# Optimization experiments

Hardware: AMD Instinct MI355X
Metric: run time of the kernel (lower is better)

The kernel has to match this reference:

```python
import jax, jax.numpy as jnp
import numpy as np

HEADS = 12
D_MODEL = 768
D_K = D_MODEL // HEADS


def setup_inputs() -> dict:
    key = jax.random.key(0)
    ks = jax.random.split(key, 5)
    B, S = 2, 2048
    scale = 1.0 / np.sqrt(D_MODEL)
    return {
        "q": jax.random.normal(ks[0], (B, S, D_MODEL), dtype=jnp.float32),
        "k": jax.random.normal(ks[1], (B, S, D_MODEL), dtype=jnp.float32),
        "v": jax.random.normal(ks[2], (B, S, D_MODEL), dtype=jnp.float32),
        "Wk": jax.random.normal(ks[3], (D_MODEL, D_MODEL), dtype=jnp.float32) * scale,
        "bk": jnp.zeros((D_MODEL,), dtype=jnp.float32),
        "Wo": jax.random.normal(ks[4], (D_MODEL, D_MODEL), dtype=jnp.float32) * scale,
        "bo": jnp.zeros((D_MODEL,), dtype=jnp.float32),
    }


def reference(q, k, v, Wk, bk, Wo, bo):
    B, S, _ = q.shape
    # NOTE: faithful to source bug: q, k, v ALL projected with k_linear.
    def proj(x):
        y = x @ Wk.T + bk                    # [B,S,D]
        return y.reshape(B, -1, HEADS, D_K).transpose(0, 2, 1, 3)  # [B,H,S,Dk]

    qh, kh, vh = proj(q), proj(k), proj(v)
    scores = jnp.einsum('bhsd,bhtd->bhst', qh, kh) / jnp.sqrt(jnp.float32(D_K))
    attn = jax.nn.softmax(scores, axis=-1)   # dropout is identity in eval
    out = jnp.einsum('bhst,bhtd->bhsd', attn, vh)
    concat = out.transpose(0, 2, 1, 3).reshape(B, -1, D_MODEL)
    return concat @ Wo.T + bo
```

## Files before the change

### kernel.cpp

```cpp
#include <hip/hip_runtime.h>
#include <hip/hip_bf16.h>
#include <stddef.h>

#define HEADS 12
#define DM 768
#define DK 64
#define SEQ 2048
#define NB 2
#define WSZ (DM * DM)
#define QSCALE 0.18033688011112043f

typedef __attribute__((ext_vector_type(8))) short short8;
typedef __attribute__((ext_vector_type(4))) float f32x4;
typedef __attribute__((ext_vector_type(16))) float f32x16;

#define MFMA16(A, B, C) __builtin_amdgcn_mfma_f32_16x16x32_bf16((A), (B), (C), 0, 0, 0)
#define MFMA32(A, B, C) __builtin_amdgcn_mfma_f32_32x32x16_bf16((A), (B), (C), 0, 0, 0)

__device__ __forceinline__ unsigned short f2bf(float x) {
  union { float f; unsigned u; } c;
  c.f = x;
  unsigned r = (c.u + 0x7FFFu + ((c.u >> 16) & 1u)) >> 16;
  return (unsigned short)r;
}
__device__ __forceinline__ float bf2f(unsigned short h) {
  union { float f; unsigned u; } c;
  c.u = ((unsigned)h) << 16;
  return c.f;
}

__device__ __forceinline__ void async16(const void* g, void* l) {
  __builtin_amdgcn_global_load_lds(
      (const __attribute__((address_space(1))) void*)g,
      (__attribute__((address_space(3))) void*)l, 16, 0, 0);
}

__device__ __forceinline__ void splitpk(float a, float b, unsigned& hu, unsigned& lu) {
  union { __hip_bfloat162 v; unsigned u; } c;
  c.v = __float22bfloat162_rn(make_float2(a, b));
  hu = c.u;
  const float ra = a - bf2f((unsigned short)(hu & 0xFFFFu));
  const float rb = b - bf2f((unsigned short)(hu >> 16));
  c.v = __float22bfloat162_rn(make_float2(ra, rb));
  lu = c.u;
}
__device__ __forceinline__ unsigned pk2bf(float a, float b) {
  union { __hip_bfloat162 v; unsigned u; } c;
  c.v = __float22bfloat162_rn(make_float2(a, b));
  return c.u;
}

__device__ __forceinline__ void pl32swap(unsigned& a, unsigned& b) {
  auto r = __builtin_amdgcn_permlane32_swap(a, b, false, false);
  a = r[0];
  b = r[1];
}


__global__ __launch_bounds__(256) void prep_split(
    const float* __restrict__ q, const float* __restrict__ k,
    const float* __restrict__ v, const float* __restrict__ Wk,
    const float* __restrict__ Wo, unsigned short* __restrict__ xq,
    unsigned short* __restrict__ xk, unsigned short* __restrict__ xv,
    unsigned short* __restrict__ wkh, unsigned short* __restrict__ wkl,
    unsigned short* __restrict__ woh, unsigned short* __restrict__ wol) {
  __shared__ __align__(16) unsigned short Lh[64 * 136];
  __shared__ __align__(16) unsigned short Ll[64 * 136];
  const int tid = threadIdx.x;
  int id = blockIdx.x;
  const float* S;
  unsigned short *H, *L = nullptr;
  int RT, RT16;
  if (id < 1152) {
    S = (id < 384) ? q : (id < 768) ? k : v;
    H = (id < 384) ? xq : (id < 768) ? xk : xv;
    id = id % 384; RT = 64; RT16 = 256;
  } else if (id < 1224) {
    S = Wk; H = wkh; L = wkl; id -= 1152; RT = 12; RT16 = 48;
  } else {
    S = Wo; H = woh; L = wol; id -= 1224; RT = 12; RT16 = 48;
  }
  const int rb = id % RT, kb = id / RT;
  const int mlane = tid >> 4;
  const int klane = (tid & 15) * 8;

#pragma unroll
  for (int rr = 0; rr < 4; ++rr) {
    const int m = rr * 16 + mlane;
    const float* src = &S[(size_t)(rb * 64 + m) * DM + kb * 128 + klane];
    float a[8];
    *(float4*)&a[0] = *(const float4*)&src[0];
    *(float4*)&a[4] = *(const float4*)&src[4];
    if (L) {
      unsigned hu[4], lu[4];
#pragma unroll
      for (int u = 0; u < 4; ++u) splitpk(a[2 * u], a[2 * u + 1], hu[u], lu[u]);
      *(uint4*)&Lh[m * 136 + klane] = *(uint4*)&hu[0];
      *(uint4*)&Ll[m * 136 + klane] = *(uint4*)&lu[0];
    } else {
      unsigned hu[4];
#pragma unroll
      for (int u = 0; u < 4; ++u) hu[u] = pk2bf(a[2 * u], a[2 * u + 1]);
      *(uint4*)&Lh[m * 136 + klane] = *(uint4*)&hu[0];
    }
  }
  __syncthreads();

  const int t = tid >> 4;
  const int ktp = t >> 2, mtp = t & 3;
  const size_t gt = ((size_t)(kb * 4 + ktp) * RT16 + (rb * 4 + mtp)) * 512;
#pragma unroll
  for (int i = 0; i < 4; ++i) {
    const int c = i * 16 + (tid & 15);
    const int lsrc = (mtp * 16 + (tid & 15)) * 136 + ktp * 32 + i * 8;
    *(uint4*)&H[gt + c * 8] = *(uint4*)&Lh[lsrc];
    if (L) *(uint4*)&L[gt + c * 8] = *(uint4*)&Ll[lsrc];
  }
}

__global__ __launch_bounds__(256, 3) void gemm_proj(
    const unsigned short* __restrict__ Xq, const unsigned short* __restrict__ Xk,
    const unsigned short* __restrict__ Xv, const unsigned short* __restrict__ Bh_,
    const unsigned short* __restrict__ Bl_, const float* __restrict__ bias,
    unsigned short* __restrict__ q_h, unsigned short* __restrict__ q_l,
    unsigned short* __restrict__ k_h, unsigned short* __restrict__ vt_h) {
  __shared__ __align__(16) unsigned short Ash[8 * 512];
  __shared__ __align__(16) unsigned short Bsh[6 * 512];
  __shared__ __align__(16) unsigned short Bsl[6 * 512];

  const int tid = threadIdx.x, z = blockIdx.z;
  const unsigned short* __restrict__ A = (z == 0) ? Xq : (z == 1) ? Xk : Xv;
  const int id = blockIdx.x;
  const int mt0 = (id & 31) * 8, nt0 = (id >> 5) * 6;
  const int lane = tid & 63, wv = tid >> 6;
  const int l15 = lane & 15, quad = lane >> 4;
  const int wm = (wv >> 1) * 4, wn = (wv & 1) * 3;
  const int lx = lane * 8;

  f32x4 acc[4][3];
#pragma unroll
  for (int i = 0; i < 4; ++i)
#pragma unroll
    for (int j = 0; j < 3; ++j) acc[i][j] = (f32x4){0.f, 0.f, 0.f, 0.f};

  for (int kt = 0; kt < 24; ++kt) {
    __syncthreads();
    async16(&A[((size_t)kt * 256 + mt0 + wv) * 512 + lx], &Ash[wv * 512]);
    async16(&A[((size_t)kt * 256 + mt0 + wv + 4) * 512 + lx], &Ash[(wv + 4) * 512]);
    async16(&Bh_[((size_t)kt * 48 + nt0 + wv) * 512 + lx], &Bsh[wv * 512]);
    async16(&Bl_[((size_t)kt * 48 + nt0 + wv) * 512 + lx], &Bsl[wv * 512]);
    if (wv < 2)
      async16(&Bh_[((size_t)kt * 48 + nt0 + 4 + wv) * 512 + lx], &Bsh[(4 + wv) * 512]);
    else
      async16(&Bl_[((size_t)kt * 48 + nt0 + 2 + wv) * 512 + lx], &Bsl[(2 + wv) * 512]);
    __syncthreads();

    short8 bh8[3], bl8[3];
#pragma unroll
    for (int nt = 0; nt < 3; ++nt) {
      bh8[nt] = *(const short8*)&Bsh[(wn + nt) * 512 + lx];
      bl8[nt] = *(const short8*)&Bsl[(wn + nt) * 512 + lx];
    }
#pragma unroll
    for (int mt = 0; mt < 4; ++mt) {
      const short8 ah8 = *(const short8*)&Ash[(wm + mt) * 512 + lx];
#pragma unroll
      for (int nt = 0; nt < 3; ++nt) {
        acc[mt][nt] = MFMA16(ah8, bh8[nt], acc[mt][nt]);
        acc[mt][nt] = MFMA16(ah8, bl8[nt], acc[mt][nt]);
      }
    }
  }

#pragma unroll
  for (int mt = 0; mt < 4; ++mt)
#pragma unroll
    for (int nt = 0; nt < 3; ++nt) {
      const int n = (nt0 + wn + nt) * 16 + l15;
      const float bv = bias[n];
      const int hh = n >> 6, dk = n & 63;
#pragma unroll
      for (int j = 0; j < 4; ++j) {
        const int m = (mt0 + wm + mt) * 16 + quad * 4 + j;
        const int b = m >> 11, t = m & 2047;
        const int bh = b * HEADS + hh;
        if (z == 0) {
          const float y = (acc[mt][nt][j] + bv) * QSCALE;
          const unsigned short yh = f2bf(y);
          const int a = (bh * SEQ + t) * DK + dk;
          q_h[a] = yh;
          q_l[a] = f2bf(y - bf2f(yh));
        } else if (z == 1) {
          const int a = bh * 131072 + (t >> 5) * 2048 + (dk >> 4) * 512 +
                        ((t & 31) + ((dk & 15) >> 3) * 32) * 8 + (dk & 7);
          k_h[a] = f2bf(acc[mt][nt][j] + bv);
        } else {
          const int a = bh * 131072 + (t >> 4) * 1024 + (dk >> 5) * 512 +
                        ((dk & 31) + ((t & 15) >> 3) * 32) * 8 + (t & 7);
          vt_h[a] = f2bf(acc[mt][nt][j] + bv);
        }
      }
    }
}

__global__ __launch_bounds__(256, 2) void gemm_out(
    const unsigned short* __restrict__ Ah_, const unsigned short* __restrict__ Al_,
    const unsigned short* __restrict__ Bh_, const unsigned short* __restrict__ Bl_,
    const float* __restrict__ bias, float* __restrict__ outF) {
  __shared__ __align__(16) unsigned short Ash[4 * 512];
  __shared__ __align__(16) unsigned short Asl[4 * 512];
  __shared__ __align__(16) unsigned short Bsh[6 * 512];
  __shared__ __align__(16) unsigned short Bsl[6 * 512];

  const int tid = threadIdx.x, id = blockIdx.x;
  const int mt0 = (id & 63) * 4, nt0 = (id >> 6) * 6;
  const int lane = tid & 63, wv = tid >> 6;
  const int l15 = lane & 15, quad = lane >> 4;
  const int wm = (wv >> 1) * 2, wn = (wv & 1) * 3;
  const int lx = lane * 8;

  f32x4 acc[2][3];
#pragma unroll
  for (int i = 0; i < 2; ++i)
#pragma unroll
    for (int j = 0; j < 3; ++j) acc[i][j] = (f32x4){0.f, 0.f, 0.f, 0.f};

  for (int kt = 0; kt < 24; ++kt) {
    __syncthreads();
    async16(&Ah_[((size_t)kt * 256 + mt0 + wv) * 512 + lx], &Ash[wv * 512]);
    async16(&Al_[((size_t)kt * 256 + mt0 + wv) * 512 + lx], &Asl[wv * 512]);
    async16(&Bh_[((size_t)kt * 48 + nt0 + wv) * 512 + lx], &Bsh[wv * 512]);
    async16(&Bl_[((size_t)kt * 48 + nt0 + wv) * 512 + lx], &Bsl[wv * 512]);
    if (wv < 2)
      async16(&Bh_[((size_t)kt * 48 + nt0 + 4 + wv) * 512 + lx], &Bsh[(4 + wv) * 512]);
    else
      async16(&Bl_[((size_t)kt * 48 + nt0 + 2 + wv) * 512 + lx], &Bsl[(2 + wv) * 512]);
    __syncthreads();

    short8 bh8[3], bl8[3];
#pragma unroll
    for (int nt = 0; nt < 3; ++nt) {
      bh8[nt] = *(const short8*)&Bsh[(wn + nt) * 512 + lx];
      bl8[nt] = *(const short8*)&Bsl[(wn + nt) * 512 + lx];
    }
#pragma unroll
    for (int mt = 0; mt < 2; ++mt) {
      const short8 ah8 = *(const short8*)&Ash[(wm + mt) * 512 + lx];
      const short8 al8 = *(const short8*)&Asl[(wm + mt) * 512 + lx];
#pragma unroll
      for (int nt = 0; nt < 3; ++nt) {
        acc[mt][nt] = MFMA16(ah8, bh8[nt], acc[mt][nt]);
        acc[mt][nt] = MFMA16(al8, bh8[nt], acc[mt][nt]);
        acc[mt][nt] = MFMA16(ah8, bl8[nt], acc[mt][nt]);
      }
    }
  }

#pragma unroll
  for (int mt = 0; mt < 2; ++mt)
#pragma unroll
    for (int nt = 0; nt < 3; ++nt) {
      const int n = (nt0 + wn + nt) * 16 + l15;
      const float bv = bias[n];
#pragma unroll
      for (int j = 0; j < 4; ++j) {
        const int m = (mt0 + wm + mt) * 16 + quad * 4 + j;
        outF[(size_t)m * DM + n] = acc[mt][nt][j] + bv;
      }
    }
}

__global__ __launch_bounds__(256, 3) void attn_mfma(
    const unsigned short* __restrict__ q_h, const unsigned short* __restrict__ q_l,
    const unsigned short* __restrict__ k_h, const unsigned short* __restrict__ vt_h,
    unsigned short* __restrict__ cch, unsigned short* __restrict__ ccl) {
  __shared__ __align__(16) union {
    unsigned short stage[32 * 512];
    float osh[64 * 64];
  } sm;
  __shared__ float Lred[4][32];

  const int tid = threadIdx.x, lane = tid & 63, wv = tid >> 6;
  const int l31 = lane & 31, hi = lane >> 5;
  const int qh = wv & 1, th = wv >> 1;
  const int id = blockIdx.x;
  const int bh = id % 24, q0 = (id / 24) << 6;
  const int lx = lane * 8;

  short8 Qf[4][2];
#pragma unroll
  for (int ks = 0; ks < 4; ++ks) {
    const int off = (bh * SEQ + q0 + qh * 32 + l31) * DK + ks * 16 + hi * 8;
    Qf[ks][0] = *(const short8*)&q_h[off];
    Qf[ks][1] = *(const short8*)&q_l[off];
  }

  f32x16 O[2];
#pragma unroll
  for (int i = 0; i < 2; ++i)
#pragma unroll
    for (int r = 0; r < 16; ++r) O[i][r] = 0.f;
  float lsum = 0.f;

  const unsigned short* __restrict__ kbh = k_h + (size_t)bh * 131072;
  const unsigned short* __restrict__ vbh = vt_h + (size_t)bh * 131072;
  unsigned short* const Ks = &sm.stage[0];
  unsigned short* const Vs = &sm.stage[16 * 512];

  for (int t0 = 0; t0 < SEQ; t0 += 128) {
    __syncthreads();
#pragma unroll
    for (int dt = 0; dt < 4; ++dt)
      async16(&kbh[((size_t)(t0 >> 5) + wv) * 2048 + dt * 512 + lx],
              &Ks[(wv * 4 + dt) * 512]);
#pragma unroll
    for (int i = 0; i < 2; ++i)
#pragma unroll
      for (int dt = 0; dt < 2; ++dt)
        async16(&vbh[((size_t)(t0 >> 4) + wv * 2 + i) * 1024 + dt * 512 + lx],
                &Vs[((wv * 2 + i) * 2 + dt) * 512]);
    __syncthreads();

    f32x16 St[2];
#pragma unroll
    for (int i = 0; i < 2; ++i)
#pragma unroll
      for (int r = 0; r < 16; ++r) St[i][r] = 0.f;
    __builtin_amdgcn_s_setprio(1);
#pragma unroll
    for (int tt = 0; tt < 2; ++tt)
#pragma unroll
      for (int ks = 0; ks < 4; ++ks) {
        const short8 kh8 =
            *(const short8*)&Ks[((th * 2 + tt) * 4 + ks) * 512 + lx];
        St[tt] = MFMA32(kh8, Qf[ks][0], St[tt]);
        St[tt] = MFMA32(kh8, Qf[ks][1], St[tt]);
      }
    __builtin_amdgcn_s_setprio(0);

#pragma unroll
    for (int tt = 0; tt < 2; ++tt) {
      float s = 0.f;
#pragma unroll
      for (int r = 0; r < 16; ++r) {
        St[tt][r] = __builtin_amdgcn_exp2f(St[tt][r]);
        s += St[tt][r];
      }
      lsum += s;
    }

    short8 pa[4];
#pragma unroll
    for (int tt = 0; tt < 2; ++tt)
#pragma unroll
      for (int c = 0; c < 2; ++c) {
        unsigned a0 = pk2bf(St[tt][c * 8 + 0], St[tt][c * 8 + 1]);
        unsigned a1 = pk2bf(St[tt][c * 8 + 2], St[tt][c * 8 + 3]);
        unsigned b0 = pk2bf(St[tt][c * 8 + 4], St[tt][c * 8 + 5]);
        unsigned b1 = pk2bf(St[tt][c * 8 + 6], St[tt][c * 8 + 7]);
        pl32swap(a0, b0);
        pl32swap(a1, b1);
        unsigned w[4] = {a0, a1, b0, b1};
        pa[tt * 2 + c] = *(short8*)&w[0];
      }

    __builtin_amdgcn_s_setprio(1);
#pragma unroll
    for (int tc = 0; tc < 4; ++tc) {
#pragma unroll
      for (int dt = 0; dt < 2; ++dt) {
        const short8 vb8 =
            *(const short8*)&Vs[((th * 4 + tc) * 2 + dt) * 512 + lx];
        O[dt] = MFMA32(pa[tc], vb8, O[dt]);
      }
    }
    __builtin_amdgcn_s_setprio(0);
  }

  {
    float l = lsum + __shfl_xor(lsum, 32);
    if (lane < 32) Lred[wv][lane] = l;
  }
  asm volatile("s_waitcnt vmcnt(0)" ::: "memory");
  __syncthreads();
  if (th == 1) {
#pragma unroll
    for (int dt = 0; dt < 2; ++dt)
#pragma unroll
      for (int r = 0; r < 16; ++r) {
        const int qloc = (r & 3) + 8 * (r >> 2) + 4 * hi;
        sm.osh[(qh * 32 + qloc) * 64 + dt * 32 + l31] = O[dt][r];
      }
  }
  __syncthreads();
  if (th == 0) {
    const int b = bh / HEADS, hh = bh % HEADS;
#pragma unroll
    for (int dt = 0; dt < 2; ++dt)
#pragma unroll
      for (int r = 0; r < 16; ++r) {
        const int qloc = (r & 3) + 8 * (r >> 2) + 4 * hi;
        const float inv = 1.0f / (Lred[qh][qloc] + Lred[qh + 2][qloc]);
        const float y =
            (O[dt][r] + sm.osh[(qh * 32 + qloc) * 64 + dt * 32 + l31]) * inv;
        const int m = b * SEQ + q0 + qh * 32 + qloc;
        const int kk = hh * 64 + dt * 32 + l31;
        const int a = ((kk >> 5) * 256 + (m >> 4)) * 512 +
                      (((kk & 31) >> 3) * 16 + (m & 15)) * 8 + (kk & 7);
        const unsigned short yh = f2bf(y);
        cch[a] = yh;
        ccl[a] = f2bf(y - bf2f(yh));
      }
  }
}

extern "C" void kernel_launch(void* const* d_in, const int* in_sizes, int n_in,
                              void* d_out, int out_size, void* d_ws,
                              size_t ws_size, hipStream_t stream) {
  const float* q = (const float*)d_in[0];
  const float* k = (const float*)d_in[1];
  const float* v = (const float*)d_in[2];
  const float* Wk = (const float*)d_in[3];
  const float* bk = (const float*)d_in[4];
  const float* Wo = (const float*)d_in[5];
  const float* bo = (const float*)d_in[6];
  float* out = (float*)d_out;

  const size_t SZ = (size_t)NB * SEQ * DM;
  unsigned short* ws16 = (unsigned short*)d_ws;
  unsigned short* xq = ws16;
  unsigned short* xk = ws16 + SZ;
  unsigned short* xv = ws16 + 2 * SZ;
  unsigned short* cch = xq;
  unsigned short* ccl = xk;
  unsigned short* qp_h = ws16 + 3 * SZ;
  unsigned short* qp_l = ws16 + 4 * SZ;
  unsigned short* kp = ws16 + 5 * SZ;
  unsigned short* vtp = ws16 + 6 * SZ;
  unsigned short* wkh = ws16 + 7 * SZ;
  unsigned short* wkl = wkh + WSZ;
  unsigned short* woh = wkl + WSZ;
  unsigned short* wol = woh + WSZ;

  prep_split<<<dim3(1296), 256, 0, stream>>>(q, k, v, Wk, Wo, xq, xk, xv, wkh,
                                             wkl, woh, wol);
  gemm_proj<<<dim3(256, 1, 3), 256, 0, stream>>>(xq, xk, xv, wkh, wkl, bk,
                                                 qp_h, qp_l, kp, vtp);
  attn_mfma<<<dim3(768), 256, 0, stream>>>(qp_h, qp_l, kp, vtp, cch, ccl);
  gemm_out<<<dim3(512), 256, 0, stream>>>(cch, ccl, woh, wol, bo, out);
}
```

Before: 195.6 us.

## Double-buffer K tiles and overlap V/K async loads with QK compute

```diff
diff --git a/kernel.cpp b/kernel.cpp
--- a/kernel.cpp
+++ b/kernel.cpp
@@ -275,7 +275,10 @@
     const unsigned short* __restrict__ k_h, const unsigned short* __restrict__ vt_h,
     unsigned short* __restrict__ cch, unsigned short* __restrict__ ccl) {
   __shared__ __align__(16) union {
-    unsigned short stage[32 * 512];
+    struct {
+      unsigned short ksb[2][16 * 512];
+      unsigned short vs[16 * 512];
+    } s;
     float osh[64 * 64];
   } sm;
   __shared__ float Lred[4][32];
@@ -304,23 +307,33 @@
 
   const unsigned short* __restrict__ kbh = k_h + (size_t)bh * 131072;
   const unsigned short* __restrict__ vbh = vt_h + (size_t)bh * 131072;
-  unsigned short* const Ks = &sm.stage[0];
-  unsigned short* const Vs = &sm.stage[16 * 512];
-
-  for (int t0 = 0; t0 < SEQ; t0 += 128) {
-    __syncthreads();
-#pragma unroll
-    for (int dt = 0; dt < 4; ++dt)
-      async16(&kbh[((size_t)(t0 >> 5) + wv) * 2048 + dt * 512 + lx],
-              &Ks[(wv * 4 + dt) * 512]);
-#pragma unroll
-    for (int i = 0; i < 2; ++i)
-#pragma unroll
-      for (int dt = 0; dt < 2; ++dt)
-        async16(&vbh[((size_t)(t0 >> 4) + wv * 2 + i) * 1024 + dt * 512 + lx],
-                &Vs[((wv * 2 + i) * 2 + dt) * 512]);
-    __syncthreads();
-
+
+#define STAGE_K(T0S, BUF)                                                      \
+  do {                                                                         \
+    _Pragma("unroll") for (int dt = 0; dt < 4; ++dt)                           \
+        async16(&kbh[(((size_t)(T0S) >> 5) + wv) * 2048 + dt * 512 + lx],      \
+                &sm.s.ksb[(BUF)][(wv * 4 + dt) * 512]);                        \
+  } while (0)
+#define STAGE_V(T0S)                                                           \
+  do {                                                                         \
+    _Pragma("unroll") for (int i = 0; i < 2; ++i)                              \
+        _Pragma("unroll") for (int dt = 0; dt < 2; ++dt)                       \
+        async16(                                                               \
+            &vbh[(((size_t)(T0S) >> 4) + wv * 2 + i) * 1024 + dt * 512 + lx],  \
+            &sm.s.vs[((wv * 2 + i) * 2 + dt) * 512]);                          \
+  } while (0)
+
+  STAGE_K(0, 0);
+  int cur = 0;
+  for (int it = 0; it < 16; ++it) {
+    const int t0 = it << 7;
+    __builtin_amdgcn_s_barrier();
+    STAGE_V(t0);
+    STAGE_K(((it + 1) & 15) << 7, cur ^ 1);
+    asm volatile("s_waitcnt vmcnt(8)" ::: "memory");
+    __builtin_amdgcn_s_barrier();
+
+    const unsigned short* Ks = &sm.s.ksb[cur][0];
     f32x16 St[2];
 #pragma unroll
     for (int i = 0; i < 2; ++i)
@@ -364,18 +377,24 @@
         pa[tt * 2 + c] = *(short8*)&w[0];
       }
 
+    asm volatile("s_waitcnt vmcnt(4)" ::: "memory");
+    __builtin_amdgcn_s_barrier();
+
     __builtin_amdgcn_s_setprio(1);
 #pragma unroll
     for (int tc = 0; tc < 4; ++tc) {
 #pragma unroll
       for (int dt = 0; dt < 2; ++dt) {
         const short8 vb8 =
-            *(const short8*)&Vs[((th * 4 + tc) * 2 + dt) * 512 + lx];
+            *(const short8*)&sm.s.vs[((th * 4 + tc) * 2 + dt) * 512 + lx];
         O[dt] = MFMA32(pa[tc], vb8, O[dt]);
       }
     }
     __builtin_amdgcn_s_setprio(0);
-  }
+    cur ^= 1;
+  }
+#undef STAGE_K
+#undef STAGE_V
 
   {
     float l = lsum + __shfl_xor(lsum, 32);
```

After: 199.3 us. About the same (+1.9%).
